# Kernel tuning notes

Hardware: AMD Instinct MI355X
Metric: run time of the kernel (lower is better)

The kernel has to match this reference:

```python
import jax, jax.numpy as jnp
import numpy as np


def setup_inputs() -> dict:
    key = jax.random.key(0)
    ks = jax.random.split(key, 12)
    N, E, D_IN, D_H, R, B, G, C, D_E = 50000, 600000, 128, 128, 8, 4, 64, 16, 16
    x = jax.random.normal(ks[0], (N, D_IN), dtype=jnp.float32)
    edge_index = jax.random.randint(ks[1], (2, E), 0, N, dtype=jnp.int64)
    edge_type = jax.random.randint(ks[2], (E,), 0, R, dtype=jnp.int64)
    edge_attr = jax.random.normal(ks[3], (E, D_E), dtype=jnp.float32)
    batch = jnp.sort(jax.random.randint(ks[4], (N,), 0, G, dtype=jnp.int64))
    # RGCNConv basis-decomposition params + root + bias
    basis = jax.random.normal(ks[5], (B, D_IN, D_H), dtype=jnp.float32) / np.sqrt(D_IN)
    comp = jax.random.normal(ks[6], (R, B), dtype=jnp.float32) / np.sqrt(B)
    root = jax.random.normal(ks[7], (D_IN, D_H), dtype=jnp.float32) / np.sqrt(D_IN)
    bias = jnp.zeros((D_H,), dtype=jnp.float32)
    fc_w = jax.random.normal(ks[8], (D_H, C), dtype=jnp.float32) / np.sqrt(D_H)
    fc_b = jnp.zeros((C,), dtype=jnp.float32)
    return {"x": x, "edge_index": edge_index, "edge_type": edge_type,
            "edge_attr": edge_attr, "batch": batch, "num_graphs": 64,
            "basis": basis, "comp": comp, "root": root, "bias": bias,
            "fc_w": fc_w, "fc_b": fc_b}


def reference(x, edge_index, edge_type, edge_attr, batch, num_graphs,
              basis, comp, root, bias, fc_w, fc_b):
    N = x.shape[0]
    R = comp.shape[0]
    src, dst = edge_index[0], edge_index[1]
    # relation weights from basis decomposition: [R, in, out]
    W = jnp.einsum('rb,bio->rio', comp, basis)
    x_src = x[src]  # gather source features [E, in]
    agg = jnp.zeros((N, W.shape[2]), dtype=x.dtype)
    # per-relation mean aggregation (PyG RGCNConv default), summed over relations
    for r in range(R):
        mask = (edge_type == r).astype(x.dtype)  # [E]
        msg = (x_src @ W[r]) * mask[:, None]     # [E, out]
        summed = jax.ops.segment_sum(msg, dst, num_segments=N)
        cnt = jax.ops.segment_sum(mask, dst, num_segments=N)
        agg = agg + summed / jnp.maximum(cnt, 1.0)[:, None]
    h = jax.nn.relu(x @ root + bias + agg)       # [N, hidden]
    # global mean pool over graphs
    pooled_sum = jax.ops.segment_sum(h, batch, num_segments=num_graphs)
    gcnt = jax.ops.segment_sum(jnp.ones((N,), dtype=x.dtype), batch, num_segments=num_graphs)
    pooled = pooled_sum / jnp.maximum(gcnt, 1.0)[:, None]  # [G, hidden]
    return pooled @ fc_w + fc_b                  # [G, num_classes]
```

## Files before the change

### kernel.cpp

```cpp
#include <hip/hip_runtime.h>

static inline int ceil_div(int a, int b){ return (a+b-1)/b; }
static inline size_t align_up(size_t x, size_t a){ return (x + a - 1) / a * a; }

typedef __bf16 bf16x8 __attribute__((ext_vector_type(8)));
typedef float  f32x4  __attribute__((ext_vector_type(4)));

static __device__ inline unsigned short f2bf(float f){
    unsigned int u = __float_as_uint(f);
    unsigned int lsb = (u >> 16) & 1u;
    u += 0x7FFFu + lsb;
    return (unsigned short)(u >> 16);
}
static __device__ inline float bf2f(unsigned short b){
    return __uint_as_float(((unsigned int)b) << 16);
}
static __device__ inline unsigned int packbf(float a, float b){
    return (unsigned int)f2bf(a) | ((unsigned int)f2bf(b) << 16);
}

static __device__ inline void gload_lds16(const void* g, void* l) {
    __builtin_amdgcn_global_load_lds(
        (const __attribute__((address_space(1))) unsigned int*)g,
        (__attribute__((address_space(3))) unsigned int*)l, 16, 0, 0);
}

__global__ __launch_bounds__(256)
void pre_kernel(const float* __restrict__ comp, const float* __restrict__ basis,
                const float* __restrict__ root, unsigned short* __restrict__ Bt, int B,
                const float* __restrict__ x, unsigned int* __restrict__ Xb2, int N,
                int* __restrict__ cnt, int NR) {
    int gtid = blockIdx.x*blockDim.x + threadIdx.x;
    int gsz  = gridDim.x*blockDim.x;
    for (int i = gtid; i < NR; i += gsz) cnt[i] = 0;
    for (int idx = gtid; idx < 128*1152; idx += gsz) {
        int o = idx / 1152, kk = idx - o*1152;
        float val;
        if (kk < 1024) {
            int r = kk >> 7, i = kk & 127;
            val = 0.f;
            for (int b = 0; b < B; ++b)
                val += comp[r*B+b] * basis[((size_t)b*128 + i)*128 + o];
        } else {
            val = root[(size_t)(kk-1024)*128 + o];
        }
        Bt[idx] = f2bf(val);
    }
    for (int tt = gtid; tt < N*64; tt += gsz) {
        int n = tt >> 6, l = tt & 63;
        float2 v = reinterpret_cast<const float2*>(x + (size_t)n*128)[l];
        Xb2[(size_t)n*64 + l] = packbf(v.x, v.y);
    }
}

__global__ void count_kernel(const int* __restrict__ dst, const int* __restrict__ et,
                             int* __restrict__ cnt, int E, int R) {
    int e = blockIdx.x*blockDim.x + threadIdx.x;
    if (e >= E) return;
    atomicAdd(&cnt[(size_t)dst[e]*R + et[e]], 1);
}

__global__ __launch_bounds__(256)
void scan_block_kernel(const int* __restrict__ in, int* __restrict__ out,
                       int* __restrict__ bsums, int n) {
    __shared__ int tsum[256];
    int t = threadIdx.x;
    int idx0 = blockIdx.x*1024 + t*4;
    int v0 = (idx0+0 < n) ? in[idx0+0] : 0;
    int v1 = (idx0+1 < n) ? in[idx0+1] : 0;
    int v2 = (idx0+2 < n) ? in[idx0+2] : 0;
    int v3 = (idx0+3 < n) ? in[idx0+3] : 0;
    int s = v0+v1+v2+v3;
    tsum[t] = s; __syncthreads();
    for (int off = 1; off < 256; off <<= 1) {
        int x = (t >= off) ? tsum[t-off] : 0;
        __syncthreads();
        tsum[t] += x;
        __syncthreads();
    }
    int run = tsum[t] - s;
    if (idx0+0 < n) out[idx0+0] = run; run += v0;
    if (idx0+1 < n) out[idx0+1] = run; run += v1;
    if (idx0+2 < n) out[idx0+2] = run; run += v2;
    if (idx0+3 < n) out[idx0+3] = run;
    if (bsums && t == 255) bsums[blockIdx.x] = tsum[255];
}

__global__ void scan_add_kernel(int* __restrict__ out, const int* __restrict__ bs,
                                int n, int total) {
    int i = blockIdx.x*blockDim.x + threadIdx.x;
    if (i < n) out[i] += bs[i >> 10];
    if (i == 0) out[n] = total;
}

__global__ void fill_kernel(const int* __restrict__ src, const int* __restrict__ dst,
                            const int* __restrict__ et, int* __restrict__ offsets,
                            int* __restrict__ slot_off, int E, int R) {
    int e = blockIdx.x*blockDim.x + threadIdx.x;
    if (e >= E) return;
    if (e < 4) slot_off[E + e] = 0;
    int bin = dst[e]*R + et[e];
    int slot = atomicAdd(&offsets[bin], 1);
    slot_off[slot] = src[e] << 6;
}

__global__ __launch_bounds__(256)
void aggregate_kernel(const int* __restrict__ offsets, const int* __restrict__ slot_off,
                      const unsigned int* __restrict__ Xb2, unsigned int* __restrict__ Mc2,
                      int N) {
    int gw = (int)((blockIdx.x*blockDim.x + threadIdx.x) >> 6);
    int node = gw >> 2, part = gw & 3;
    if (node >= N) return;
    int l = threadIdx.x & 63;
    int base = node*8 + part*2;
    int lo   = (base == 0) ? 0 : offsets[base-1];
    int bmid = offsets[base];
    int hi   = offsets[base+1];

    float ax0=0.f, ay0=0.f, ax1=0.f, ay1=0.f;

#define ACC2(E_, U_) { \
    float vx_ = bf2f((unsigned short)((U_) & 0xFFFFu)); \
    float vy_ = bf2f((unsigned short)((U_) >> 16)); \
    if ((E_) < bmid) { ax0 += vx_; ay0 += vy_; } \
    else             { ax1 += vx_; ay1 += vy_; } }

    for (int e = lo; e < hi; e += 4) {
        int s0 = slot_off[e];
        int s1 = slot_off[e+1];
        int s2 = slot_off[e+2];
        int s3 = slot_off[e+3];
        unsigned int u0 = Xb2[(unsigned)(s0 + l)];
        unsigned int u1 = Xb2[(unsigned)(s1 + l)];
        unsigned int u2 = Xb2[(unsigned)(s2 + l)];
        unsigned int u3 = Xb2[(unsigned)(s3 + l)];
        if (e+1 >= hi) u1 = 0u;
        if (e+2 >= hi) u2 = 0u;
        if (e+3 >= hi) u3 = 0u;
        ACC2(e+0, u0) ACC2(e+1, u1) ACC2(e+2, u2) ACC2(e+3, u3)
    }
#undef ACC2

    unsigned int* Mrow = Mc2 + (size_t)node*512;
    float i0 = 1.f/fmaxf((float)(bmid-lo), 1.f);
    float i1 = 1.f/fmaxf((float)(hi-bmid), 1.f);
    __builtin_nontemporal_store(packbf(ax0*i0, ay0*i0), &Mrow[(2*part+0)*64 + l]);
    __builtin_nontemporal_store(packbf(ax1*i1, ay1*i1), &Mrow[(2*part+1)*64 + l]);
}

__global__ __launch_bounds__(256)
void mfma_gemm_kernel(const unsigned short* __restrict__ Mc,
                      const unsigned short* __restrict__ Xb,
                      const unsigned short* __restrict__ Btc,
                      const float* __restrict__ bias,
                      unsigned short* __restrict__ h, int MBrows) {
    __shared__ char ldsA[64*128];
    __shared__ char ldsB[64*128];

    int tid  = threadIdx.x;
    int lane = tid & 63;
    int wid  = tid >> 6;
    int rg = wid & 1, cg = wid >> 1;
    int fr = lane & 15, kb = lane >> 4;

    int blk = blockIdx.x;
    int q = blk >> 4, rem = blk & 15, c = rem >> 3, m = rem & 7;
    int rb = q*8 + m;
    if (rb >= MBrows) return;
    long m0 = (long)rb * 64;
    int colbase = c * 64;

    int lrow8 = lane >> 3;
    int lcb   = (lane & 7) * 16;

    f32x4 acc[2][2];
    #pragma unroll
    for (int mf = 0; mf < 2; ++mf)
        #pragma unroll
        for (int nf = 0; nf < 2; ++nf) acc[mf][nf] = f32x4{0.f,0.f,0.f,0.f};

    const char* McB = (const char*)Mc;
    const char* XbB = (const char*)Xb;
    const char* BtB = (const char*)Btc;

    for (int t = 0; t < 18; ++t) {
        #pragma unroll
        for (int i = 0; i < 2; ++i) {
            int row = wid*16 + i*8 + lrow8;
            int sw  = lcb ^ ((row & 7) << 4);
            const char* g = (t < 16)
                ? McB + (size_t)(m0 + row)*2048 + t*128 + sw
                : XbB + (size_t)(m0 + row)*256 + (t-16)*128 + sw;
            gload_lds16(g, &ldsA[wid*2048 + i*1024 + lane*16]);
        }
        #pragma unroll
        for (int i = 0; i < 2; ++i) {
            int col = wid*16 + i*8 + lrow8;
            int sw  = lcb ^ ((col & 7) << 4);
            const char* g = BtB + (size_t)(colbase + col)*2304 + t*128 + sw;
            gload_lds16(g, &ldsB[wid*2048 + i*1024 + lane*16]);
        }
        __syncthreads();

        bf16x8 af[2][2], bfr[2][2];
        #pragma unroll
        for (int mf = 0; mf < 2; ++mf) {
            int row = rg*32 + mf*16 + fr;
            #pragma unroll
            for (int kk = 0; kk < 2; ++kk) {
                int byte = row*128 + ((kk*64 + kb*16) ^ ((row & 7) << 4));
                af[mf][kk] = *reinterpret_cast<const bf16x8*>(&ldsA[byte]);
            }
        }
        #pragma unroll
        for (int nf = 0; nf < 2; ++nf) {
            int col = cg*32 + nf*16 + fr;
            #pragma unroll
            for (int kk = 0; kk < 2; ++kk) {
                int byte = col*128 + ((kk*64 + kb*16) ^ ((col & 7) << 4));
                bfr[nf][kk] = *reinterpret_cast<const bf16x8*>(&ldsB[byte]);
            }
        }
        #pragma unroll
        for (int kk = 0; kk < 2; ++kk)
            #pragma unroll
            for (int mf = 0; mf < 2; ++mf)
                #pragma unroll
                for (int nf = 0; nf < 2; ++nf)
                    acc[mf][nf] = __builtin_amdgcn_mfma_f32_16x16x32_bf16(
                        af[mf][kk], bfr[nf][kk], acc[mf][nf], 0, 0, 0);
        __syncthreads();
    }

    float bb[2];
    #pragma unroll
    for (int nf = 0; nf < 2; ++nf) bb[nf] = bias[colbase + cg*32 + nf*16 + fr];

    #pragma unroll
    for (int mf = 0; mf < 2; ++mf)
        #pragma unroll
        for (int q2 = 0; q2 < 4; ++q2) {
            long r = m0 + rg*32 + mf*16 + kb*4 + q2;
            unsigned short* hr = h + (size_t)r*128 + colbase + cg*32;
            #pragma unroll
            for (int nf = 0; nf < 2; ++nf)
                hr[nf*16 + fr] = f2bf(fmaxf(acc[mf][nf][q2] + bb[nf], 0.f));
        }
}

__global__ __launch_bounds__(512)
void pool_fc_kernel(const unsigned int* __restrict__ h2, const int* __restrict__ batch,
                    const float* __restrict__ fw, const float* __restrict__ fb,
                    float* __restrict__ out, int N, int C) {
    int g = blockIdx.x;
    int t = threadIdx.x;
    int lo = 0, hi = N;
    while (lo < hi) { int mid = (lo+hi) >> 1; if (batch[mid] < g) lo = mid+1; else hi = mid; }
    int s0 = lo;
    hi = N;
    while (lo < hi) { int mid = (lo+hi) >> 1; if (batch[mid] < g+1) lo = mid+1; else hi = mid; }
    int s1 = lo;

    int d2 = t & 63;
    float ax = 0.f, ay = 0.f;
    for (int row = s0 + (t >> 6); row < s1; row += 8) {
        unsigned int u = h2[(size_t)row*64 + d2];
        ax += bf2f((unsigned short)(u & 0xFFFFu));
        ay += bf2f((unsigned short)(u >> 16));
    }
    __shared__ float ps[128];
    if (t < 128) ps[t] = 0.f;
    __syncthreads();
    atomicAdd(&ps[2*d2],   ax);
    atomicAdd(&ps[2*d2+1], ay);
    __syncthreads();
    if (t < C) {
        float inv = 1.f / fmaxf((float)(s1 - s0), 1.f);
        float s = 0.f;
        #pragma unroll 4
        for (int k = 0; k < 128; ++k) s += ps[k] * fw[(size_t)k*C + t];
        out[(size_t)g*C + t] = s * inv + fb[t];
    }
}

extern "C" void kernel_launch(void* const* d_in, const int* in_sizes, int n_in,
                              void* d_out, int out_size, void* d_ws, size_t ws_size,
                              hipStream_t stream) {
    const float* x       = (const float*)d_in[0];
    const int*   eindex  = (const int*)  d_in[1];
    const int*   etype   = (const int*)  d_in[2];
    const int*   batch   = (const int*)  d_in[4];
    const float* basis   = (const float*)d_in[6];
    const float* comp    = (const float*)d_in[7];
    const float* root    = (const float*)d_in[8];
    const float* bias    = (const float*)d_in[9];
    const float* fc_w    = (const float*)d_in[10];
    const float* fc_b    = (const float*)d_in[11];

    int N  = in_sizes[4];
    int E  = in_sizes[2];
    int C  = in_sizes[11];
    int G  = out_size / C;
    int IO = in_sizes[8];
    int B  = in_sizes[6] / IO;
    int R  = in_sizes[7] / B;
    int NR = N * R;
    int MB = ceil_div(N, 64);
    int Mpad = MB * 64;
    int grid_gemm = ceil_div(MB, 8) * 16;

    const int* src = eindex;
    const int* dst = eindex + E;

    char* base = (char*)d_ws;
    size_t off = 0;
    auto alloc = [&](size_t bytes) -> char* {
        char* p = base + off;
        off = align_up(off + bytes, 256);
        return p;
    };
    unsigned short* Bt  = (unsigned short*)alloc(sizeof(unsigned short)*128*1152);
    int*   cnt      = (int*)  alloc(sizeof(int)*(size_t)NR);
    int*   offsets  = (int*)  alloc(sizeof(int)*((size_t)NR+1));
    int*   bsums    = (int*)  alloc(sizeof(int)*1024);
    int*   slot_off = (int*)  alloc(sizeof(int)*((size_t)E+4));
    unsigned short* h  = (unsigned short*)alloc(sizeof(unsigned short)*(size_t)Mpad*128);
    unsigned short* Xb = (unsigned short*)alloc(sizeof(unsigned short)*(size_t)Mpad*128);
    unsigned short* Mc = (unsigned short*)alloc(sizeof(unsigned short)*(size_t)Mpad*1024);

    pre_kernel<<<1024,256,0,stream>>>(comp, basis, root, Bt, B,
                                      x, (unsigned int*)Xb, N, cnt, NR);
    count_kernel<<<ceil_div(E,256),256,0,stream>>>(dst, etype, cnt, E, R);

    int nb = ceil_div(NR, 1024);
    scan_block_kernel<<<nb,256,0,stream>>>(cnt, offsets, bsums, NR);
    scan_block_kernel<<<1,256,0,stream>>>(bsums, bsums, nullptr, nb);
    scan_add_kernel<<<ceil_div(NR,256),256,0,stream>>>(offsets, bsums, NR, E);

    fill_kernel<<<ceil_div(E,256),256,0,stream>>>(src, dst, etype, offsets, slot_off, E, R);

    aggregate_kernel<<<ceil_div(N*4*64,256),256,0,stream>>>(offsets, slot_off,
                                                            (const unsigned int*)Xb,
                                                            (unsigned int*)Mc, N);

    mfma_gemm_kernel<<<grid_gemm,256,0,stream>>>(Mc, Xb, Bt, bias, h, MB);

    pool_fc_kernel<<<G,512,0,stream>>>((const unsigned int*)h, batch, fc_w, fc_b,
                                       (float*)d_out, N, C);
}
```

Measured before the change: 213.5 us.

## Inline up to three source offsets per bin for direct aggregation

The fill kernel now also records each bin's count and its first three source offsets in a per-bin int4, using an atomic decrement on the count array to rank edges. For bins with three or fewer edges, which is nearly all of them at an average of about 1.5 edges per bin, the aggregate kernel reads this record and gathers the rows directly, skipping the offsets and slot_off indirection. In exchange the fill kernel does an extra atomic and scattered writes, and there is a new 16-byte-per-bin buffer to write and read.

New measurement: 261.5 us. 22.5% more time.

```diff
diff --git a/kernel.cpp b/kernel.cpp
--- a/kernel.cpp
+++ b/kernel.cpp
@@ -62,7 +62,7 @@
 
 __global__ __launch_bounds__(256)
 void scan_block_kernel(const int* __restrict__ in, int* __restrict__ out,
-                       int* __restrict__ bsums, int n) {
+                       int* __restrict__ bsums, int4* __restrict__ binfo, int n) {
     __shared__ int tsum[256];
     int t = threadIdx.x;
     int idx0 = blockIdx.x*1024 + t*4;
@@ -70,6 +70,12 @@
     int v1 = (idx0+1 < n) ? in[idx0+1] : 0;
     int v2 = (idx0+2 < n) ? in[idx0+2] : 0;
     int v3 = (idx0+3 < n) ? in[idx0+3] : 0;
+    if (binfo) {
+        if (idx0+0 < n) binfo[idx0+0] = make_int4(v0,0,0,0);
+        if (idx0+1 < n) binfo[idx0+1] = make_int4(v1,0,0,0);
+        if (idx0+2 < n) binfo[idx0+2] = make_int4(v2,0,0,0);
+        if (idx0+3 < n) binfo[idx0+3] = make_int4(v3,0,0,0);
+    }
     int s = v0+v1+v2+v3;
     tsum[t] = s; __syncthreads();
     for (int off = 1; off < 256; off <<= 1) {
@@ -95,17 +101,23 @@
 
 __global__ void fill_kernel(const int* __restrict__ src, const int* __restrict__ dst,
                             const int* __restrict__ et, int* __restrict__ offsets,
+                            int* __restrict__ cnt, int4* __restrict__ binfo,
                             int* __restrict__ slot_off, int E, int R) {
     int e = blockIdx.x*blockDim.x + threadIdx.x;
     if (e >= E) return;
     if (e < 4) slot_off[E + e] = 0;
     int bin = dst[e]*R + et[e];
+    int soff = src[e] << 6;
     int slot = atomicAdd(&offsets[bin], 1);
-    slot_off[slot] = src[e] << 6;
+    slot_off[slot] = soff;
+    int rank_rev = atomicSub(&cnt[bin], 1);
+    int rank = binfo[bin].x - rank_rev;
+    if (rank < 3) ((int*)&binfo[bin])[1 + rank] = soff;
 }
 
 __global__ __launch_bounds__(256)
 void aggregate_kernel(const int* __restrict__ offsets, const int* __restrict__ slot_off,
+                      const int4* __restrict__ binfo,
                       const unsigned int* __restrict__ Xb2, unsigned int* __restrict__ Mc2,
                       int N) {
     int gw = (int)((blockIdx.x*blockDim.x + threadIdx.x) >> 6);
@@ -113,39 +125,55 @@
     if (node >= N) return;
     int l = threadIdx.x & 63;
     int base = node*8 + part*2;
-    int lo   = (base == 0) ? 0 : offsets[base-1];
-    int bmid = offsets[base];
-    int hi   = offsets[base+1];
-
-    float ax0=0.f, ay0=0.f, ax1=0.f, ay1=0.f;
-
-#define ACC2(E_, U_) { \
-    float vx_ = bf2f((unsigned short)((U_) & 0xFFFFu)); \
-    float vy_ = bf2f((unsigned short)((U_) >> 16)); \
-    if ((E_) < bmid) { ax0 += vx_; ay0 += vy_; } \
-    else             { ax1 += vx_; ay1 += vy_; } }
-
-    for (int e = lo; e < hi; e += 4) {
-        int s0 = slot_off[e];
-        int s1 = slot_off[e+1];
-        int s2 = slot_off[e+2];
-        int s3 = slot_off[e+3];
-        unsigned int u0 = Xb2[(unsigned)(s0 + l)];
-        unsigned int u1 = Xb2[(unsigned)(s1 + l)];
-        unsigned int u2 = Xb2[(unsigned)(s2 + l)];
-        unsigned int u3 = Xb2[(unsigned)(s3 + l)];
-        if (e+1 >= hi) u1 = 0u;
-        if (e+2 >= hi) u2 = 0u;
-        if (e+3 >= hi) u3 = 0u;
-        ACC2(e+0, u0) ACC2(e+1, u1) ACC2(e+2, u2) ACC2(e+3, u3)
-    }
-#undef ACC2
+
+    unsigned int res[2];
+
+    #pragma unroll
+    for (int bb = 0; bb < 2; ++bb) {
+        int bin = base + bb;
+        int4 bi = binfo[bin];
+        int cnt = bi.x;
+        float ax, ay;
+        if (cnt <= 3) {
+            unsigned int u0 = Xb2[(unsigned)(bi.y + l)];
+            unsigned int u1 = Xb2[(unsigned)(bi.z + l)];
+            unsigned int u2 = Xb2[(unsigned)(bi.w + l)];
+            if (cnt < 1) u0 = 0u;
+            if (cnt < 2) u1 = 0u;
+            if (cnt < 3) u2 = 0u;
+            ax = __uint_as_float(u0 << 16) + __uint_as_float(u1 << 16)
+               + __uint_as_float(u2 << 16);
+            ay = __uint_as_float(u0 & 0xFFFF0000u) + __uint_as_float(u1 & 0xFFFF0000u)
+               + __uint_as_float(u2 & 0xFFFF0000u);
+        } else {
+            int lo = (bin == 0) ? 0 : offsets[bin-1];
+            int hi = offsets[bin];
+            ax = 0.f; ay = 0.f;
+            for (int e = lo; e < hi; e += 4) {
+                int s0 = slot_off[e];
+                int s1 = slot_off[e+1];
+                int s2 = slot_off[e+2];
+                int s3 = slot_off[e+3];
+                unsigned int u0 = Xb2[(unsigned)(s0 + l)];
+                unsigned int u1 = Xb2[(unsigned)(s1 + l)];
+                unsigned int u2 = Xb2[(unsigned)(s2 + l)];
+                unsigned int u3 = Xb2[(unsigned)(s3 + l)];
+                if (e+1 >= hi) u1 = 0u;
+                if (e+2 >= hi) u2 = 0u;
+                if (e+3 >= hi) u3 = 0u;
+                ax += __uint_as_float(u0 << 16) + __uint_as_float(u1 << 16)
+                    + __uint_as_float(u2 << 16) + __uint_as_float(u3 << 16);
+                ay += __uint_as_float(u0 & 0xFFFF0000u) + __uint_as_float(u1 & 0xFFFF0000u)
+                    + __uint_as_float(u2 & 0xFFFF0000u) + __uint_as_float(u3 & 0xFFFF0000u);
+            }
+        }
+        float inv = 1.f / fmaxf((float)cnt, 1.f);
+        res[bb] = packbf(ax*inv, ay*inv);
+    }
 
     unsigned int* Mrow = Mc2 + (size_t)node*512;
-    float i0 = 1.f/fmaxf((float)(bmid-lo), 1.f);
-    float i1 = 1.f/fmaxf((float)(hi-bmid), 1.f);
-    __builtin_nontemporal_store(packbf(ax0*i0, ay0*i0), &Mrow[(2*part+0)*64 + l]);
-    __builtin_nontemporal_store(packbf(ax1*i1, ay1*i1), &Mrow[(2*part+1)*64 + l]);
+    __builtin_nontemporal_store(res[0], &Mrow[(2*part+0)*64 + l]);
+    __builtin_nontemporal_store(res[1], &Mrow[(2*part+1)*64 + l]);
 }
 
 __global__ __launch_bounds__(256)
@@ -323,6 +351,7 @@
     int*   cnt      = (int*)  alloc(sizeof(int)*(size_t)NR);
     int*   offsets  = (int*)  alloc(sizeof(int)*((size_t)NR+1));
     int*   bsums    = (int*)  alloc(sizeof(int)*1024);
+    int4*  binfo    = (int4*) alloc(sizeof(int4)*(size_t)NR);
     int*   slot_off = (int*)  alloc(sizeof(int)*((size_t)E+4));
     unsigned short* h  = (unsigned short*)alloc(sizeof(unsigned short)*(size_t)Mpad*128);
     unsigned short* Xb = (unsigned short*)alloc(sizeof(unsigned short)*(size_t)Mpad*128);
@@ -333,13 +362,14 @@
     count_kernel<<<ceil_div(E,256),256,0,stream>>>(dst, etype, cnt, E, R);
 
     int nb = ceil_div(NR, 1024);
-    scan_block_kernel<<<nb,256,0,stream>>>(cnt, offsets, bsums, NR);
-    scan_block_kernel<<<1,256,0,stream>>>(bsums, bsums, nullptr, nb);
+    scan_block_kernel<<<nb,256,0,stream>>>(cnt, offsets, bsums, binfo, NR);
+    scan_block_kernel<<<1,256,0,stream>>>(bsums, bsums, nullptr, nullptr, nb);
     scan_add_kernel<<<ceil_div(NR,256),256,0,stream>>>(offsets, bsums, NR, E);
 
-    fill_kernel<<<ceil_div(E,256),256,0,stream>>>(src, dst, etype, offsets, slot_off, E, R);
-
-    aggregate_kernel<<<ceil_div(N*4*64,256),256,0,stream>>>(offsets, slot_off,
+    fill_kernel<<<ceil_div(E,256),256,0,stream>>>(src, dst, etype, offsets, cnt, binfo,
+                                                  slot_off, E, R);
+
+    aggregate_kernel<<<ceil_div(N*4*64,256),256,0,stream>>>(offsets, slot_off, binfo,
                                                             (const unsigned int*)Xb,
                                                             (unsigned int*)Mc, N);
 
```

## Double-buffer LDS tiles in MFMA GEMM to overlap loads with compute

Applied to the files above, without the earlier changes.

Splits the LDS A/B tiles into two buffers and prefetches the next k-step with direct global-to-LDS loads while the current buffer is consumed by MFMA. Per-step __syncthreads are replaced with explicit vmcnt waits and raw barriers, so global memory latency is meant to hide behind compute. It doubles LDS use per block, which may lower occupancy, and relies on hand-written waitcnt counts being correct.

Result: no change. 213.6 us (+0.0%).

```diff
diff --git a/kernel.cpp b/kernel.cpp
--- a/kernel.cpp
+++ b/kernel.cpp
@@ -154,8 +154,8 @@
                       const unsigned short* __restrict__ Btc,
                       const float* __restrict__ bias,
                       unsigned short* __restrict__ h, int MBrows) {
-    __shared__ char ldsA[64*128];
-    __shared__ char ldsB[64*128];
+    __shared__ char ldsA[2][64*128];
+    __shared__ char ldsB[2][64*128];
 
     int tid  = threadIdx.x;
     int lane = tid & 63;
@@ -183,7 +183,7 @@
     const char* XbB = (const char*)Xb;
     const char* BtB = (const char*)Btc;
 
-    for (int t = 0; t < 18; ++t) {
+    auto stage = [&](int t, int buf) {
         #pragma unroll
         for (int i = 0; i < 2; ++i) {
             int row = wid*16 + i*8 + lrow8;
@@ -191,16 +191,32 @@
             const char* g = (t < 16)
                 ? McB + (size_t)(m0 + row)*2048 + t*128 + sw
                 : XbB + (size_t)(m0 + row)*256 + (t-16)*128 + sw;
-            gload_lds16(g, &ldsA[wid*2048 + i*1024 + lane*16]);
+            gload_lds16(g, &ldsA[buf][wid*2048 + i*1024 + lane*16]);
         }
         #pragma unroll
         for (int i = 0; i < 2; ++i) {
             int col = wid*16 + i*8 + lrow8;
             int sw  = lcb ^ ((col & 7) << 4);
             const char* g = BtB + (size_t)(colbase + col)*2304 + t*128 + sw;
-            gload_lds16(g, &ldsB[wid*2048 + i*1024 + lane*16]);
-        }
-        __syncthreads();
+            gload_lds16(g, &ldsB[buf][wid*2048 + i*1024 + lane*16]);
+        }
+    };
+
+    stage(0, 0);
+    asm volatile("s_waitcnt vmcnt(0)" ::: "memory");
+    __builtin_amdgcn_s_barrier();
+
+    for (int t = 0; t < 18; ++t) {
+        int cur = t & 1;
+        if (t + 1 < 18) {
+            stage(t + 1, cur ^ 1);
+            asm volatile("s_waitcnt vmcnt(4)" ::: "memory");
+        } else {
+            asm volatile("s_waitcnt vmcnt(0)" ::: "memory");
+        }
+        __builtin_amdgcn_sched_barrier(0);
+        __builtin_amdgcn_s_barrier();
+        __builtin_amdgcn_sched_barrier(0);
 
         bf16x8 af[2][2], bfr[2][2];
         #pragma unroll
@@ -209,7 +225,7 @@
             #pragma unroll
             for (int kk = 0; kk < 2; ++kk) {
                 int byte = row*128 + ((kk*64 + kb*16) ^ ((row & 7) << 4));
-                af[mf][kk] = *reinterpret_cast<const bf16x8*>(&ldsA[byte]);
+                af[mf][kk] = *reinterpret_cast<const bf16x8*>(&ldsA[cur][byte]);
             }
         }
         #pragma unroll
@@ -218,7 +234,7 @@
             #pragma unroll
             for (int kk = 0; kk < 2; ++kk) {
                 int byte = col*128 + ((kk*64 + kb*16) ^ ((col & 7) << 4));
-                bfr[nf][kk] = *reinterpret_cast<const bf16x8*>(&ldsB[byte]);
+                bfr[nf][kk] = *reinterpret_cast<const bf16x8*>(&ldsB[cur][byte]);
             }
         }
         #pragma unroll
@@ -229,7 +245,9 @@
                 for (int nf = 0; nf < 2; ++nf)
                     acc[mf][nf] = __builtin_amdgcn_mfma_f32_16x16x32_bf16(
                         af[mf][kk], bfr[nf][kk], acc[mf][nf], 0, 0, 0);
-        __syncthreads();
+
+        __builtin_amdgcn_sched_barrier(0);
+        __builtin_amdgcn_s_barrier();
     }
 
     float bb[2];
```

## Fuse mean-pool into GEMM epilogue via atomics and double-buffer LDS tiles

Applied to the files above, without the earlier changes.

The GEMM epilogue now stages ReLU outputs in shared memory and accumulates per-graph column sums directly into a global psum buffer with atomics. This removes the bf16 h write-back and the separate pool kernel's reread of h. A small fc_kernel then applies the mean and the FC layer. LDS tiles are also split into two alternating buffers, though the loop still synchronises twice per step, so overlap is limited. The changes also keep pooled values in fp32 rather than bf16, and add atomic contention on a small G×128 buffer.

After: 193.4 us. -9.4%, faster.

```diff
diff --git a/kernel.cpp b/kernel.cpp
--- a/kernel.cpp
+++ b/kernel.cpp
@@ -29,10 +29,11 @@
 void pre_kernel(const float* __restrict__ comp, const float* __restrict__ basis,
                 const float* __restrict__ root, unsigned short* __restrict__ Bt, int B,
                 const float* __restrict__ x, unsigned int* __restrict__ Xb2, int N,
-                int* __restrict__ cnt, int NR) {
+                int* __restrict__ cnt, int NR, float* __restrict__ psum, int G) {
     int gtid = blockIdx.x*blockDim.x + threadIdx.x;
     int gsz  = gridDim.x*blockDim.x;
     for (int i = gtid; i < NR; i += gsz) cnt[i] = 0;
+    for (int i = gtid; i < G*128; i += gsz) psum[i] = 0.f;
     for (int idx = gtid; idx < 128*1152; idx += gsz) {
         int o = idx / 1152, kk = idx - o*1152;
         float val;
@@ -153,9 +154,11 @@
                       const unsigned short* __restrict__ Xb,
                       const unsigned short* __restrict__ Btc,
                       const float* __restrict__ bias,
-                      unsigned short* __restrict__ h, int MBrows) {
-    __shared__ char ldsA[64*128];
-    __shared__ char ldsB[64*128];
+                      const int* __restrict__ batch,
+                      float* __restrict__ psum, int Nrows, int MBrows) {
+    __shared__ char ldsRaw[32768];
+    auto ldsA = [&](int buf) -> char* { return ldsRaw + buf*8192; };
+    auto ldsB = [&](int buf) -> char* { return ldsRaw + 16384 + buf*8192; };
 
     int tid  = threadIdx.x;
     int lane = tid & 63;
@@ -184,6 +187,7 @@
     const char* BtB = (const char*)Btc;
 
     for (int t = 0; t < 18; ++t) {
+        int cur = t & 1;
         #pragma unroll
         for (int i = 0; i < 2; ++i) {
             int row = wid*16 + i*8 + lrow8;
@@ -191,14 +195,14 @@
             const char* g = (t < 16)
                 ? McB + (size_t)(m0 + row)*2048 + t*128 + sw
                 : XbB + (size_t)(m0 + row)*256 + (t-16)*128 + sw;
-            gload_lds16(g, &ldsA[wid*2048 + i*1024 + lane*16]);
+            gload_lds16(g, ldsA(cur) + wid*2048 + i*1024 + lane*16);
         }
         #pragma unroll
         for (int i = 0; i < 2; ++i) {
             int col = wid*16 + i*8 + lrow8;
             int sw  = lcb ^ ((col & 7) << 4);
             const char* g = BtB + (size_t)(colbase + col)*2304 + t*128 + sw;
-            gload_lds16(g, &ldsB[wid*2048 + i*1024 + lane*16]);
+            gload_lds16(g, ldsB(cur) + wid*2048 + i*1024 + lane*16);
         }
         __syncthreads();
 
@@ -209,7 +213,7 @@
             #pragma unroll
             for (int kk = 0; kk < 2; ++kk) {
                 int byte = row*128 + ((kk*64 + kb*16) ^ ((row & 7) << 4));
-                af[mf][kk] = *reinterpret_cast<const bf16x8*>(&ldsA[byte]);
+                af[mf][kk] = *reinterpret_cast<const bf16x8*>(ldsA(cur) + byte);
             }
         }
         #pragma unroll
@@ -218,7 +222,7 @@
             #pragma unroll
             for (int kk = 0; kk < 2; ++kk) {
                 int byte = col*128 + ((kk*64 + kb*16) ^ ((col & 7) << 4));
-                bfr[nf][kk] = *reinterpret_cast<const bf16x8*>(&ldsB[byte]);
+                bfr[nf][kk] = *reinterpret_cast<const bf16x8*>(ldsB(cur) + byte);
             }
         }
         #pragma unroll
@@ -236,51 +240,53 @@
     #pragma unroll
     for (int nf = 0; nf < 2; ++nf) bb[nf] = bias[colbase + cg*32 + nf*16 + fr];
 
+    float* ldsF = (float*)ldsRaw;
     #pragma unroll
     for (int mf = 0; mf < 2; ++mf)
         #pragma unroll
         for (int q2 = 0; q2 < 4; ++q2) {
-            long r = m0 + rg*32 + mf*16 + kb*4 + q2;
-            unsigned short* hr = h + (size_t)r*128 + colbase + cg*32;
+            int rl = rg*32 + mf*16 + kb*4 + q2;
             #pragma unroll
-            for (int nf = 0; nf < 2; ++nf)
-                hr[nf*16 + fr] = f2bf(fmaxf(acc[mf][nf][q2] + bb[nf], 0.f));
-        }
-}
-
-__global__ __launch_bounds__(512)
-void pool_fc_kernel(const unsigned int* __restrict__ h2, const int* __restrict__ batch,
-                    const float* __restrict__ fw, const float* __restrict__ fb,
-                    float* __restrict__ out, int N, int C) {
-    int g = blockIdx.x;
-    int t = threadIdx.x;
+            for (int nf = 0; nf < 2; ++nf) {
+                int cl = cg*32 + nf*16 + fr;
+                ldsF[rl*66 + cl] = fmaxf(acc[mf][nf][q2] + bb[nf], 0.f);
+            }
+        }
+    __syncthreads();
+
+    int col = tid & 63, rq = tid >> 6;
+    float partial = 0.f;
+    int gcur = -1;
+    for (int i = 0; i < 16; ++i) {
+        long row = m0 + rq*16 + i;
+        if (row >= Nrows) break;
+        int g = batch[row];
+        if (g != gcur) {
+            if (gcur >= 0) atomicAdd(&psum[(size_t)gcur*128 + colbase + col], partial);
+            gcur = g; partial = 0.f;
+        }
+        partial += ldsF[(rq*16 + i)*66 + col];
+    }
+    if (gcur >= 0) atomicAdd(&psum[(size_t)gcur*128 + colbase + col], partial);
+}
+
+__global__ void fc_kernel(const float* __restrict__ psum, const int* __restrict__ batch,
+                          const float* __restrict__ fw, const float* __restrict__ fb,
+                          float* __restrict__ out, int N, int G, int C) {
+    int idx = blockIdx.x*blockDim.x + threadIdx.x;
+    if (idx >= G*C) return;
+    int g = idx / C, cc = idx - g*C;
     int lo = 0, hi = N;
     while (lo < hi) { int mid = (lo+hi) >> 1; if (batch[mid] < g) lo = mid+1; else hi = mid; }
     int s0 = lo;
     hi = N;
     while (lo < hi) { int mid = (lo+hi) >> 1; if (batch[mid] < g+1) lo = mid+1; else hi = mid; }
-    int s1 = lo;
-
-    int d2 = t & 63;
-    float ax = 0.f, ay = 0.f;
-    for (int row = s0 + (t >> 6); row < s1; row += 8) {
-        unsigned int u = h2[(size_t)row*64 + d2];
-        ax += bf2f((unsigned short)(u & 0xFFFFu));
-        ay += bf2f((unsigned short)(u >> 16));
-    }
-    __shared__ float ps[128];
-    if (t < 128) ps[t] = 0.f;
-    __syncthreads();
-    atomicAdd(&ps[2*d2],   ax);
-    atomicAdd(&ps[2*d2+1], ay);
-    __syncthreads();
-    if (t < C) {
-        float inv = 1.f / fmaxf((float)(s1 - s0), 1.f);
-        float s = 0.f;
-        #pragma unroll 4
-        for (int k = 0; k < 128; ++k) s += ps[k] * fw[(size_t)k*C + t];
-        out[(size_t)g*C + t] = s * inv + fb[t];
-    }
+    float inv = 1.f / fmaxf((float)(lo - s0), 1.f);
+    float s = fb[cc];
+    #pragma unroll 4
+    for (int k = 0; k < 128; ++k)
+        s += psum[(size_t)g*128 + k] * inv * fw[(size_t)k*C + cc];
+    out[idx] = s;
 }
 
 extern "C" void kernel_launch(void* const* d_in, const int* in_sizes, int n_in,
@@ -324,12 +330,12 @@
     int*   offsets  = (int*)  alloc(sizeof(int)*((size_t)NR+1));
     int*   bsums    = (int*)  alloc(sizeof(int)*1024);
     int*   slot_off = (int*)  alloc(sizeof(int)*((size_t)E+4));
-    unsigned short* h  = (unsigned short*)alloc(sizeof(unsigned short)*(size_t)Mpad*128);
+    float* psum     = (float*)alloc(sizeof(float)*(size_t)G*128);
     unsigned short* Xb = (unsigned short*)alloc(sizeof(unsigned short)*(size_t)Mpad*128);
     unsigned short* Mc = (unsigned short*)alloc(sizeof(unsigned short)*(size_t)Mpad*1024);
 
     pre_kernel<<<1024,256,0,stream>>>(comp, basis, root, Bt, B,
-                                      x, (unsigned int*)Xb, N, cnt, NR);
+                                      x, (unsigned int*)Xb, N, cnt, NR, psum, G);
     count_kernel<<<ceil_div(E,256),256,0,stream>>>(dst, etype, cnt, E, R);
 
     int nb = ceil_div(NR, 1024);
@@ -343,8 +349,8 @@
                                                             (const unsigned int*)Xb,
                                                             (unsigned int*)Mc, N);
 
-    mfma_gemm_kernel<<<grid_gemm,256,0,stream>>>(Mc, Xb, Bt, bias, h, MB);
-
-    pool_fc_kernel<<<G,512,0,stream>>>((const unsigned int*)h, batch, fc_w, fc_b,
-                                       (float*)d_out, N, C);
-}
+    mfma_gemm_kernel<<<grid_gemm,256,0,stream>>>(Mc, Xb, Bt, bias, batch, psum, N, MB);
+
+    fc_kernel<<<ceil_div(G*C,256),256,0,stream>>>(psum, batch, fc_w, fc_b,
+                                                  (float*)d_out, N, G, C);
+}
```
